# Optimization experiments

Measured on AMD Instinct MI355X. Metric: run time of the kernel, lower is better.

## Reference

```python
import jax, jax.numpy as jnp
import numpy as np

NEG_SLOPE = 0.01  # F.leaky_relu default
EPS = 1e-12       # F.normalize default eps

def _lrelu(h):
    return jnp.where(h > 0, h, NEG_SLOPE * h)

def setup_inputs() -> dict:
    key = jax.random.key(0)
    ks = jax.random.split(key, 16)
    N, E, D = 100000, 800000, 64
    x = jax.random.normal(ks[0], (N, D), dtype=jnp.float32)
    src = jax.random.randint(ks[1], (E,), 0, N, dtype=jnp.int32)
    dst = jax.random.randint(ks[2], (E,), 0, N, dtype=jnp.int32)
    def lin(k, fo, fi):
        k1, k2 = jax.random.split(k)
        s = 1.0 / np.sqrt(fi)
        w = jax.random.uniform(k1, (fo, fi), jnp.float32, -s, s)
        b = jax.random.uniform(k2, (fo,), jnp.float32, -s, s)
        return w, b
    w1, b1 = lin(ks[3], 256, D)
    w2, b2 = lin(ks[4], 128, 256)
    w3, b3 = lin(ks[5], 64, 128)
    w4, b4 = lin(ks[6], 1, 64)
    w_self, _ = lin(ks[7], D, D)   # SAGEConv fc_self (no bias)
    w_neigh, _ = lin(ks[8], D, D)  # SAGEConv fc_neigh (no bias)
    bias = jnp.zeros((D,), jnp.float32)  # SAGEConv bias param
    return dict(x=x, src=src, dst=dst, w1=w1, b1=b1, w2=w2, b2=b2,
                w3=w3, b3=b3, w4=w4, b4=b4,
                w_self=w_self, w_neigh=w_neigh, bias=bias)

def reference(x, src, dst, w1, b1, w2, b2, w3, b3, w4, b4, w_self, w_neigh, bias):
    N = x.shape[0]
    # per-edge score MLP on (h_u - h_v)
    d = x[src] - x[dst]                       # [E, D]
    h = _lrelu(d @ w1.T + b1)                 # [E, 256]
    h = _lrelu(h @ w2.T + b2)                 # [E, 128]
    h = _lrelu(h @ w3.T + b3)                 # [E, 64]
    e = jax.nn.sigmoid(h @ w4.T + b4)         # [E, 1]
    # SAGEConv 'mean' with edge weights: mean over incoming edges of e * x_src
    msg = e * x[src]                          # [E, D]
    s = jax.ops.segment_sum(msg, dst, num_segments=N)               # [N, D]
    deg = jax.ops.segment_sum(jnp.ones((src.shape[0],), x.dtype), dst,
                              num_segments=N)                        # [N]
    neigh = s / jnp.maximum(deg, 1.0)[:, None]
    A = x @ w_self.T + neigh @ w_neigh.T + bias
    A = _lrelu(A)
    norm = jnp.maximum(jnp.linalg.norm(A, axis=1, keepdims=True), EPS)
    A = A / norm
    return A, e
```

## Files before the change

kernel.cpp:

```cpp
#include <hip/hip_runtime.h>
#include <hip/hip_bf16.h>

typedef unsigned short u16;
typedef unsigned int   u32;
typedef __attribute__((ext_vector_type(8))) short short8;
typedef __attribute__((ext_vector_type(4))) float f32x4;

__device__ __forceinline__ u16 f2bf(float f) {
  u32 u = __float_as_uint(f);
  u += 0x7FFFu + ((u >> 16) & 1u);
  return (u16)(u >> 16);
}
__device__ __forceinline__ float bf2f(u16 h) { return __uint_as_float(((u32)h) << 16); }
__device__ __forceinline__ u32 pk2(float lo, float hi) {
  union { __hip_bfloat162 h; u32 u; } c;
  c.h = __float22bfloat162_rn(make_float2(lo, hi));
  return c.u;
}
__device__ __forceinline__ float lrelu(float v) { return v > 0.f ? v : 0.01f * v; }

__host__ __device__ __forceinline__ int sig(int c) {
  return ((c >> 5) << 5) | ((c & 12) << 1) | (((c >> 4) & 1) << 2) | (c & 3);
}

union U8 { u32 w[4]; short8 v; };

#define MFMA16(A, B, C) __builtin_amdgcn_mfma_f32_16x16x32_bf16(A, B, C, 0, 0, 0)

#define W2_BASE 2048
#define W3_BASE 6144
#define NCHUNK8 7168


__global__ __launch_bounds__(512, 1) void edge_mlp(
    const float* __restrict__ x, const int* __restrict__ src, const int* __restrict__ dst,
    const short8* __restrict__ wcat,
    const float* __restrict__ b1p, const float* __restrict__ b2p, const float* __restrict__ b3p,
    const float* __restrict__ w4p, const float* __restrict__ b4,
    const int* __restrict__ rowptr, const int* __restrict__ ord,
    u16* __restrict__ msgbuf, float* __restrict__ eout, int E)
{
  __shared__ short8 ldsw[NCHUNK8];
  const int tid  = threadIdx.x;
  const int lane = tid & 63;
  const int wv   = tid >> 6;
  const int g    = lane >> 4;
  const int r    = lane & 15;
  const int eb   = (blockIdx.x * 8 + wv) * 64;
  const float b4v = b4[0];

  int e[4], ec[4], sn[4], dn[4], pos[4];
#pragma unroll
  for (int c = 0; c < 4; c++) {
    e[c]  = eb + 16 * c + r;
    ec[c] = e[c] < E ? e[c] : E - 1;
    sn[c] = src[ec[c]];
    dn[c] = dst[ec[c]];
  }

  float4 xs[4][4], xd[4][4];
#pragma unroll
  for (int c = 0; c < 4; c++) {
    const float* xsr = x + (size_t)sn[c] * 64 + 8 * g;
    const float* xdr = x + (size_t)dn[c] * 64 + 8 * g;
    xs[c][0] = *(const float4*)(xsr);      xs[c][1] = *(const float4*)(xsr + 4);
    xs[c][2] = *(const float4*)(xsr + 32); xs[c][3] = *(const float4*)(xsr + 36);
    xd[c][0] = *(const float4*)(xdr);      xd[c][1] = *(const float4*)(xdr + 4);
    xd[c][2] = *(const float4*)(xdr + 32); xd[c][3] = *(const float4*)(xdr + 36);
  }
#pragma unroll
  for (int c = 0; c < 4; c++) pos[c] = rowptr[dn[c]] + ord[ec[c]];

  {
    const short8* gp = wcat + wv * 64 + lane;
    short8*       lp = ldsw + wv * 64;
#pragma unroll
    for (int i = 0; i < 14; i++) {
      __builtin_amdgcn_global_load_lds(
          (const __attribute__((address_space(1))) u32*)(gp + i * 512),
          (__attribute__((address_space(3))) u32*)(lp + i * 512), 16, 0, 0);
    }
  }
  __syncthreads();

  U8 bA[4], bB[4];
#pragma unroll
  for (int c = 0; c < 4; c++) {
    bA[c].w[0] = pk2(xs[c][0].x - xd[c][0].x, xs[c][0].y - xd[c][0].y);
    bA[c].w[1] = pk2(xs[c][0].z - xd[c][0].z, xs[c][0].w - xd[c][0].w);
    bA[c].w[2] = pk2(xs[c][1].x - xd[c][1].x, xs[c][1].y - xd[c][1].y);
    bA[c].w[3] = pk2(xs[c][1].z - xd[c][1].z, xs[c][1].w - xd[c][1].w);
    bB[c].w[0] = pk2(xs[c][2].x - xd[c][2].x, xs[c][2].y - xd[c][2].y);
    bB[c].w[1] = pk2(xs[c][2].z - xd[c][2].z, xs[c][2].w - xd[c][2].w);
    bB[c].w[2] = pk2(xs[c][3].x - xd[c][3].x, xs[c][3].y - xd[c][3].y);
    bB[c].w[3] = pk2(xs[c][3].z - xd[c][3].z, xs[c][3].w - xd[c][3].w);
  }

  U8 h1[4][8];
  {
    const float* b1l = b1p + 4 * g;
#pragma unroll
    for (int t = 0; t < 16; t++) {
      short8 a0 = ldsw[(t * 2 + 0) * 64 + lane];
      short8 a1 = ldsw[(t * 2 + 1) * 64 + lane];
      float4 bb = *(const float4*)(b1l + 16 * t);
      const int w0 = 2 * t, w1 = 2 * t + 1;
#pragma unroll
      for (int c = 0; c < 4; c++) {
        f32x4 p = {};
        p = MFMA16(a0, bA[c].v, p);
        p = MFMA16(a1, bB[c].v, p);
        h1[c][w0 >> 2].w[w0 & 3] = pk2(lrelu(p[0] + bb.x), lrelu(p[1] + bb.y));
        h1[c][w1 >> 2].w[w1 & 3] = pk2(lrelu(p[2] + bb.z), lrelu(p[3] + bb.w));
      }
    }
  }

  U8 h2[4][4];
  {
    const float* b2l = b2p + 4 * g;
#pragma unroll
    for (int t = 0; t < 8; t++) {
      f32x4 p0 = {}, p1 = {}, p2 = {}, p3 = {};
#pragma unroll
      for (int s = 0; s < 8; s++) {
        short8 a = ldsw[W2_BASE + (t * 8 + s) * 64 + lane];
        p0 = MFMA16(a, h1[0][s].v, p0);
        p1 = MFMA16(a, h1[1][s].v, p1);
        p2 = MFMA16(a, h1[2][s].v, p2);
        p3 = MFMA16(a, h1[3][s].v, p3);
      }
      float4 bb = *(const float4*)(b2l + 16 * t);
      const int w0 = 2 * t, w1 = 2 * t + 1;
      h2[0][w0 >> 2].w[w0 & 3] = pk2(lrelu(p0[0] + bb.x), lrelu(p0[1] + bb.y));
      h2[0][w1 >> 2].w[w1 & 3] = pk2(lrelu(p0[2] + bb.z), lrelu(p0[3] + bb.w));
      h2[1][w0 >> 2].w[w0 & 3] = pk2(lrelu(p1[0] + bb.x), lrelu(p1[1] + bb.y));
      h2[1][w1 >> 2].w[w1 & 3] = pk2(lrelu(p1[2] + bb.z), lrelu(p1[3] + bb.w));
      h2[2][w0 >> 2].w[w0 & 3] = pk2(lrelu(p2[0] + bb.x), lrelu(p2[1] + bb.y));
      h2[2][w1 >> 2].w[w1 & 3] = pk2(lrelu(p2[2] + bb.z), lrelu(p2[3] + bb.w));
      h2[3][w0 >> 2].w[w0 & 3] = pk2(lrelu(p3[0] + bb.x), lrelu(p3[1] + bb.y));
      h2[3][w1 >> 2].w[w1 & 3] = pk2(lrelu(p3[2] + bb.z), lrelu(p3[3] + bb.w));
    }
  }

  float dot[4] = {0.f, 0.f, 0.f, 0.f};
  {
    const float* b3l = b3p + 4 * g;
    const float* w4l = w4p + 4 * g;
#pragma unroll
    for (int t = 0; t < 4; t++) {
      f32x4 p0 = {}, p1 = {}, p2 = {}, p3 = {};
#pragma unroll
      for (int s = 0; s < 4; s++) {
        short8 a = ldsw[W3_BASE + (t * 4 + s) * 64 + lane];
        p0 = MFMA16(a, h2[0][s].v, p0);
        p1 = MFMA16(a, h2[1][s].v, p1);
        p2 = MFMA16(a, h2[2][s].v, p2);
        p3 = MFMA16(a, h2[3][s].v, p3);
      }
      float4 bb = *(const float4*)(b3l + 16 * t);
      float4 ww = *(const float4*)(w4l + 16 * t);
      dot[0] += lrelu(p0[0] + bb.x) * ww.x + lrelu(p0[1] + bb.y) * ww.y
              + lrelu(p0[2] + bb.z) * ww.z + lrelu(p0[3] + bb.w) * ww.w;
      dot[1] += lrelu(p1[0] + bb.x) * ww.x + lrelu(p1[1] + bb.y) * ww.y
              + lrelu(p1[2] + bb.z) * ww.z + lrelu(p1[3] + bb.w) * ww.w;
      dot[2] += lrelu(p2[0] + bb.x) * ww.x + lrelu(p2[1] + bb.y) * ww.y
              + lrelu(p2[2] + bb.z) * ww.z + lrelu(p2[3] + bb.w) * ww.w;
      dot[3] += lrelu(p3[0] + bb.x) * ww.x + lrelu(p3[1] + bb.y) * ww.y
              + lrelu(p3[2] + bb.z) * ww.z + lrelu(p3[3] + bb.w) * ww.w;
    }
  }
  float ev[4];
#pragma unroll
  for (int c = 0; c < 4; c++) {
    float d = dot[c];
    d += __shfl_xor(d, 16);
    d += __shfl_xor(d, 32);
    ev[c] = 1.f / (1.f + __expf(-(d + b4v)));
  }

  if (g == 0) {
#pragma unroll
    for (int c = 0; c < 4; c++)
      if (e[c] < E) eout[e[c]] = ev[c];
  }
#pragma unroll
  for (int c = 0; c < 4; c++) {
    if (e[c] < E) {
      const float* xsr = x + (size_t)sn[c] * 64 + 8 * g;
      const float4 v0 = *(const float4*)(xsr);
      const float4 v1 = *(const float4*)(xsr + 4);
      const float4 v2 = *(const float4*)(xsr + 32);
      const float4 v3 = *(const float4*)(xsr + 36);
      u16* mp = msgbuf + (size_t)pos[c] * 64 + g * 16;
      U8 m;
      m.w[0] = pk2(ev[c] * v0.x, ev[c] * v0.y);
      m.w[1] = pk2(ev[c] * v0.z, ev[c] * v0.w);
      m.w[2] = pk2(ev[c] * v1.x, ev[c] * v1.y);
      m.w[3] = pk2(ev[c] * v1.z, ev[c] * v1.w);
      *(short8*)(mp) = m.v;
      m.w[0] = pk2(ev[c] * v2.x, ev[c] * v2.y);
      m.w[1] = pk2(ev[c] * v2.z, ev[c] * v2.w);
      m.w[2] = pk2(ev[c] * v3.x, ev[c] * v3.y);
      m.w[3] = pk2(ev[c] * v3.z, ev[c] * v3.w);
      *(short8*)(mp + 8) = m.v;
    }
  }
}

__global__ void deg_hist(const int* __restrict__ dst, int* __restrict__ degi,
                         int* __restrict__ ord, int E)
{
  const int i = blockIdx.x * 256 + threadIdx.x;
  if (i < E) ord[i] = atomicAdd(&degi[dst[i]], 1);
}

__global__ void scan_part(const int* __restrict__ degi, int* __restrict__ rowptr,
                          int* __restrict__ bsum, int N)
{
  __shared__ int wsum[4];
  const int tid = threadIdx.x, lane = tid & 63, w = tid >> 6;
  const int base = blockIdx.x * 1024 + tid * 4;
  int d0 = 0, d1 = 0, d2 = 0, d3 = 0;
  if (base + 3 < N) {
    int4 v = *(const int4*)(degi + base);
    d0 = v.x; d1 = v.y; d2 = v.z; d3 = v.w;
  } else {
    if (base < N)     d0 = degi[base];
    if (base + 1 < N) d1 = degi[base + 1];
    if (base + 2 < N) d2 = degi[base + 2];
    if (base + 3 < N) d3 = degi[base + 3];
  }
  const int ts = d0 + d1 + d2 + d3;
  int sc = ts;
#pragma unroll
  for (int o = 1; o < 64; o <<= 1) { int v = __shfl_up(sc, o); if (lane >= o) sc += v; }
  if (lane == 63) wsum[w] = sc;
  __syncthreads();
  int woff = 0;
  for (int i = 0; i < w; i++) woff += wsum[i];
  const int ex = woff + sc - ts;
  if (base < N)     rowptr[base]     = ex;
  if (base + 1 < N) rowptr[base + 1] = ex + d0;
  if (base + 2 < N) rowptr[base + 2] = ex + d0 + d1;
  if (base + 3 < N) rowptr[base + 3] = ex + d0 + d1 + d2;
  if (tid == 255) bsum[blockIdx.x] = woff + sc;
}

__global__ void scan_bsum(int* __restrict__ bsum, int nb)
{
  __shared__ int wsum[4];
  const int tid = threadIdx.x, lane = tid & 63, w = tid >> 6;
  const int v = tid < nb ? bsum[tid] : 0;
  int sc = v;
#pragma unroll
  for (int o = 1; o < 64; o <<= 1) { int t = __shfl_up(sc, o); if (lane >= o) sc += t; }
  if (lane == 63) wsum[w] = sc;
  __syncthreads();
  int woff = 0;
  for (int i = 0; i < w; i++) woff += wsum[i];
  if (tid < nb) bsum[tid] = woff + sc - v;
}

__global__ void scan_add(int* __restrict__ rowptr, const int* __restrict__ bsum,
                         int N, int E)
{
  const int base = blockIdx.x * 1024 + threadIdx.x * 4;
  const int off = bsum[blockIdx.x];
#pragma unroll
  for (int i = 0; i < 4; i++)
    if (base + i < N) rowptr[base + i] += off;
  if (blockIdx.x == 0 && threadIdx.x == 0) rowptr[N] = E;
}

__global__ __launch_bounds__(256, 4) void node_agg_mfma(
    const float* __restrict__ x, const u16* __restrict__ msgbuf,
    const int* __restrict__ rowptr, const short8* __restrict__ wfin,
    const float* __restrict__ bias, float* __restrict__ A, int N)
{
  __shared__ short8 ldsW[1024];
  __shared__ float  nbuf[4][16][68];
  const int tid = threadIdx.x, wv = tid >> 6, lane = tid & 63;
  const int g = lane >> 4, r = lane & 15;
  for (int i = tid; i < 1024; i += 256) ldsW[i] = wfin[i];

  const int n0 = (blockIdx.x * 4 + wv) * 16;
  const int nr = (n0 + r) < N ? (n0 + r) : N - 1;
  const float* xp = x + (size_t)nr * 64 + 8 * g;
  const float4 xf0 = *(const float4*)(xp);
  const float4 xf1 = *(const float4*)(xp + 4);
  const float4 xf2 = *(const float4*)(xp + 32);
  const float4 xf3 = *(const float4*)(xp + 36);
  int rp = 0;
  if (lane < 17) rp = rowptr[min(n0 + lane, N)];
  const int cch = (((lane >> 3) & 1) << 5) | ((lane >> 4) << 3) | (lane & 7);
  for (int rr = 0; rr < 16; rr++) {
    const int s = __shfl(rp, rr);
    const int t = __shfl(rp, rr + 1);
    float acc = 0.f;
    for (int j = s; j < t; j += 4) {
      const int j1 = (j + 1 < t) ? j + 1 : j;
      const int j2 = (j + 2 < t) ? j + 2 : j;
      const int j3 = (j + 3 < t) ? j + 3 : j;
      const float v0 = bf2f(msgbuf[(size_t)j  * 64 + lane]);
      const float v1 = bf2f(msgbuf[(size_t)j1 * 64 + lane]);
      const float v2 = bf2f(msgbuf[(size_t)j2 * 64 + lane]);
      const float v3 = bf2f(msgbuf[(size_t)j3 * 64 + lane]);
      const float m1 = (j + 1 < t) ? 1.f : 0.f;
      const float m2 = (j + 2 < t) ? 1.f : 0.f;
      const float m3 = (j + 3 < t) ? 1.f : 0.f;
      acc += v0 + m1 * v1 + m2 * v2 + m3 * v3;
    }
    const float inv = 1.f / fmaxf((float)(t - s), 1.f);
    nbuf[wv][rr][cch] = acc * inv;
  }
  __syncthreads();

  U8 bf0, bf1, bf2q, bf3q;
  bf0.w[0] = pk2(xf0.x, xf0.y); bf0.w[1] = pk2(xf0.z, xf0.w);
  bf0.w[2] = pk2(xf1.x, xf1.y); bf0.w[3] = pk2(xf1.z, xf1.w);
  bf1.w[0] = pk2(xf2.x, xf2.y); bf1.w[1] = pk2(xf2.z, xf2.w);
  bf1.w[2] = pk2(xf3.x, xf3.y); bf1.w[3] = pk2(xf3.z, xf3.w);
  {
    const float* nb = nbuf[wv][r];
    const float4 n0v = *(const float4*)(nb + 8 * g);
    const float4 n1v = *(const float4*)(nb + 8 * g + 4);
    const float4 n2v = *(const float4*)(nb + 32 + 8 * g);
    const float4 n3v = *(const float4*)(nb + 32 + 8 * g + 4);
    bf2q.w[0] = pk2(n0v.x, n0v.y); bf2q.w[1] = pk2(n0v.z, n0v.w);
    bf2q.w[2] = pk2(n1v.x, n1v.y); bf2q.w[3] = pk2(n1v.z, n1v.w);
    bf3q.w[0] = pk2(n2v.x, n2v.y); bf3q.w[1] = pk2(n2v.z, n2v.w);
    bf3q.w[2] = pk2(n3v.x, n3v.y); bf3q.w[3] = pk2(n3v.z, n3v.w);
  }

  f32x4 acct[4] = {};
#pragma unroll
  for (int t = 0; t < 4; t++) {
    acct[t] = MFMA16(ldsW[(t * 4 + 0) * 64 + lane], bf0.v,  acct[t]);
    acct[t] = MFMA16(ldsW[(t * 4 + 1) * 64 + lane], bf1.v,  acct[t]);
    acct[t] = MFMA16(ldsW[(t * 4 + 2) * 64 + lane], bf2q.v, acct[t]);
    acct[t] = MFMA16(ldsW[(t * 4 + 3) * 64 + lane], bf3q.v, acct[t]);
  }

  f32x4 av[4];
  float ss = 0.f;
#pragma unroll
  for (int t = 0; t < 4; t++) {
    const float4 bb = *(const float4*)(bias + 16 * t + 4 * g);
    av[t][0] = lrelu(acct[t][0] + bb.x);
    av[t][1] = lrelu(acct[t][1] + bb.y);
    av[t][2] = lrelu(acct[t][2] + bb.z);
    av[t][3] = lrelu(acct[t][3] + bb.w);
    ss += av[t][0] * av[t][0] + av[t][1] * av[t][1]
        + av[t][2] * av[t][2] + av[t][3] * av[t][3];
  }
  ss += __shfl_xor(ss, 16); ss += __shfl_xor(ss, 32);
  const float rn = 1.f / fmaxf(sqrtf(ss), 1e-12f);
  if (n0 + r < N) {
    float* ap = A + (size_t)(n0 + r) * 64 + 4 * g;
#pragma unroll
    for (int t = 0; t < 4; t++) {
      float4 o;
      o.x = av[t][0] * rn; o.y = av[t][1] * rn;
      o.z = av[t][2] * rn; o.w = av[t][3] * rn;
      *(float4*)(ap + 16 * t) = o;
    }
  }
}

__global__ void convert_w(const float* __restrict__ w1, const float* __restrict__ w2,
                          const float* __restrict__ w3,
                          const float* __restrict__ b1, const float* __restrict__ b2,
                          const float* __restrict__ b3, const float* __restrict__ w4,
                          const float* __restrict__ w_self, const float* __restrict__ w_neigh,
                          u16* __restrict__ wcat, u16* __restrict__ wfin,
                          float* __restrict__ b1p, float* __restrict__ b2p,
                          float* __restrict__ b3p, float* __restrict__ w4p)
{
  const int idx = blockIdx.x * 256 + threadIdx.x;
  if (idx < 57344) {
    const float* w; int K, nsteps, loc;
    if (idx < 16384)      { loc = idx;         w = w1; K = 64;  nsteps = 2; }
    else if (idx < 49152) { loc = idx - 16384; w = w2; K = 256; nsteps = 8; }
    else                  { loc = idx - 49152; w = w3; K = 128; nsteps = 4; }
    const int chunk = loc >> 9;
    const int lane  = (loc >> 3) & 63;
    const int j     = loc & 7;
    const int t = chunk / nsteps, s = chunk % nsteps;
    const int m = sig(t * 16 + (lane & 15));
    const int k = s * 32 + (lane >> 4) * 8 + j;
    wcat[idx] = f2bf(w[m * K + k]);
  } else if (idx < 65536) {
    const int o = idx - 57344;
    const int c = o >> 9, lane = (o >> 3) & 63, j = o & 7;
    const int t = c >> 2, s = c & 3;
    const int m = 16 * t + (lane & 15);
    const int k = 32 * s + ((lane >> 4) << 3) + j;
    wfin[o] = f2bf(k < 64 ? w_self[m * 64 + k] : w_neigh[m * 64 + (k - 64)]);
  }
  if (idx < 256) b1p[idx] = b1[sig(idx)];
  if (idx < 128) b2p[idx] = b2[sig(idx)];
  if (idx < 64)  { b3p[idx] = b3[sig(idx)]; w4p[idx] = w4[sig(idx)]; }
}

extern "C" void kernel_launch(void* const* d_in, const int* in_sizes, int n_in,
                              void* d_out, int out_size, void* d_ws, size_t ws_size,
                              hipStream_t stream)
{
  const float* x       = (const float*)d_in[0];
  const int*   src     = (const int*)d_in[1];
  const int*   dst     = (const int*)d_in[2];
  const float* w1      = (const float*)d_in[3];
  const float* b1      = (const float*)d_in[4];
  const float* w2      = (const float*)d_in[5];
  const float* b2      = (const float*)d_in[6];
  const float* w3      = (const float*)d_in[7];
  const float* b3      = (const float*)d_in[8];
  const float* w4      = (const float*)d_in[9];
  const float* b4      = (const float*)d_in[10];
  const float* w_self  = (const float*)d_in[11];
  const float* w_neigh = (const float*)d_in[12];
  const float* bias    = (const float*)d_in[13];

  const int N = in_sizes[0] / 64;
  const int E = in_sizes[1];

  float* A    = (float*)d_out;
  float* eout = (float*)d_out + (size_t)N * 64;

  char* ws = (char*)d_ws;
  size_t off = 0;
  auto alloc = [&](size_t bytes) {
    void* p = ws + off;
    off = (off + bytes + 255) & ~(size_t)255;
    return p;
  };
  int*    degi   = (int*)alloc((size_t)N * 4);
  int*    rowptr = (int*)alloc((size_t)(N + 1) * 4);
  int*    ord    = (int*)alloc((size_t)E * 4);
  int*    bsum   = (int*)alloc(1024 * 4);
  short8* wcat   = (short8*)alloc((size_t)57344 * 2);
  short8* wfin   = (short8*)alloc((size_t)8192 * 2);
  float*  b1p    = (float*)alloc(256 * 4);
  float*  b2p    = (float*)alloc(128 * 4);
  float*  b3p    = (float*)alloc(64 * 4);
  float*  w4p    = (float*)alloc(64 * 4);
  u16*    msgbuf = (u16*)alloc((size_t)E * 128);

  hipMemsetAsync(degi, 0, (size_t)N * sizeof(int), stream);

  convert_w<<<256, 256, 0, stream>>>(w1, w2, w3, b1, b2, b3, w4, w_self, w_neigh,
                                     (u16*)wcat, (u16*)wfin, b1p, b2p, b3p, w4p);

  deg_hist<<<(E + 255) / 256, 256, 0, stream>>>(dst, degi, ord, E);

  const int nsb = (N + 1023) / 1024;
  scan_part<<<nsb, 256, 0, stream>>>(degi, rowptr, bsum, N);
  scan_bsum<<<1, 256, 0, stream>>>(bsum, nsb);
  scan_add<<<nsb, 256, 0, stream>>>(rowptr, bsum, N, E);

  const int nblk = (E + 511) / 512;
  edge_mlp<<<nblk, 512, 0, stream>>>(x, src, dst, wcat, b1p, b2p, b3p, w4p, b4,
                                     rowptr, ord, msgbuf, eout, E);

  const int nblk2 = (N + 63) / 64;
  node_agg_mfma<<<nblk2, 256, 0, stream>>>(x, msgbuf, rowptr, wfin, bias, A, N);
}
```

Measured before the change: 305.3 us.

## Stream MLP weights from global memory with register prefetch instead of LDS staging

Removes the per-block staging of all MLP weights into shared memory and the block barrier. Each wave now reads weight fragments straight from global memory (L2/L1-cached), prefetching the next fragment into registers while the current MFMAs run. Block size drops from 512 to 256 threads. Biases are folded into the MFMA accumulator initialisation, and leaky ReLU becomes a fmax. The trade is more global/L1 traffic per wave and extra register pressure, in exchange for no LDS fill or barrier and a smaller block that may allow more resident blocks.

```diff
diff --git a/kernel.cpp b/kernel.cpp
--- a/kernel.cpp
+++ b/kernel.cpp
@@ -17,7 +17,7 @@
   c.h = __float22bfloat162_rn(make_float2(lo, hi));
   return c.u;
 }
-__device__ __forceinline__ float lrelu(float v) { return v > 0.f ? v : 0.01f * v; }
+__device__ __forceinline__ float lrelu(float v) { return fmaxf(v, 0.01f * v); }
 
 __host__ __device__ __forceinline__ int sig(int c) {
   return ((c >> 5) << 5) | ((c & 12) << 1) | (((c >> 4) & 1) << 2) | (c & 3);
@@ -29,10 +29,9 @@
 
 #define W2_BASE 2048
 #define W3_BASE 6144
-#define NCHUNK8 7168
-
-
-__global__ __launch_bounds__(512, 1) void edge_mlp(
+
+
+__global__ __launch_bounds__(256, 1) void edge_mlp(
     const float* __restrict__ x, const int* __restrict__ src, const int* __restrict__ dst,
     const short8* __restrict__ wcat,
     const float* __restrict__ b1p, const float* __restrict__ b2p, const float* __restrict__ b3p,
@@ -40,13 +39,12 @@
     const int* __restrict__ rowptr, const int* __restrict__ ord,
     u16* __restrict__ msgbuf, float* __restrict__ eout, int E)
 {
-  __shared__ short8 ldsw[NCHUNK8];
   const int tid  = threadIdx.x;
   const int lane = tid & 63;
   const int wv   = tid >> 6;
   const int g    = lane >> 4;
   const int r    = lane & 15;
-  const int eb   = (blockIdx.x * 8 + wv) * 64;
+  const int eb   = (blockIdx.x * 4 + wv) * 64;
   const float b4v = b4[0];
 
   int e[4], ec[4], sn[4], dn[4], pos[4];
@@ -71,17 +69,8 @@
 #pragma unroll
   for (int c = 0; c < 4; c++) pos[c] = rowptr[dn[c]] + ord[ec[c]];
 
-  {
-    const short8* gp = wcat + wv * 64 + lane;
-    short8*       lp = ldsw + wv * 64;
-#pragma unroll
-    for (int i = 0; i < 14; i++) {
-      __builtin_amdgcn_global_load_lds(
-          (const __attribute__((address_space(1))) u32*)(gp + i * 512),
-          (__attribute__((address_space(3))) u32*)(lp + i * 512), 16, 0, 0);
-    }
-  }
-  __syncthreads();
+  short8 w1f0 = wcat[lane];
+  short8 w1f1 = wcat[64 + lane];
 
   U8 bA[4], bB[4];
 #pragma unroll
@@ -101,73 +90,90 @@
     const float* b1l = b1p + 4 * g;
 #pragma unroll
     for (int t = 0; t < 16; t++) {
-      short8 a0 = ldsw[(t * 2 + 0) * 64 + lane];
-      short8 a1 = ldsw[(t * 2 + 1) * 64 + lane];
+      short8 a0 = w1f0, a1 = w1f1;
+      if (t < 15) {
+        w1f0 = wcat[(2 * t + 2) * 64 + lane];
+        w1f1 = wcat[(2 * t + 3) * 64 + lane];
+      }
       float4 bb = *(const float4*)(b1l + 16 * t);
       const int w0 = 2 * t, w1 = 2 * t + 1;
 #pragma unroll
       for (int c = 0; c < 4; c++) {
-        f32x4 p = {};
+        f32x4 p = {bb.x, bb.y, bb.z, bb.w};
         p = MFMA16(a0, bA[c].v, p);
         p = MFMA16(a1, bB[c].v, p);
-        h1[c][w0 >> 2].w[w0 & 3] = pk2(lrelu(p[0] + bb.x), lrelu(p[1] + bb.y));
-        h1[c][w1 >> 2].w[w1 & 3] = pk2(lrelu(p[2] + bb.z), lrelu(p[3] + bb.w));
+        h1[c][w0 >> 2].w[w0 & 3] = pk2(lrelu(p[0]), lrelu(p[1]));
+        h1[c][w1 >> 2].w[w1 & 3] = pk2(lrelu(p[2]), lrelu(p[3]));
       }
     }
   }
 
   U8 h2[4][4];
   {
+    short8 wf0 = wcat[W2_BASE + lane];
+    short8 wf1 = wcat[W2_BASE + 64 + lane];
     const float* b2l = b2p + 4 * g;
 #pragma unroll
     for (int t = 0; t < 8; t++) {
-      f32x4 p0 = {}, p1 = {}, p2 = {}, p3 = {};
-#pragma unroll
-      for (int s = 0; s < 8; s++) {
-        short8 a = ldsw[W2_BASE + (t * 8 + s) * 64 + lane];
-        p0 = MFMA16(a, h1[0][s].v, p0);
-        p1 = MFMA16(a, h1[1][s].v, p1);
-        p2 = MFMA16(a, h1[2][s].v, p2);
-        p3 = MFMA16(a, h1[3][s].v, p3);
+      float4 bb = *(const float4*)(b2l + 16 * t);
+      f32x4 p0 = {bb.x, bb.y, bb.z, bb.w};
+      f32x4 p1 = p0, p2 = p0, p3 = p0;
+#pragma unroll
+      for (int s = 0; s < 8; s += 2) {
+        const int f = t * 8 + s;
+        short8 a0 = wf0, a1 = wf1;
+        if (f + 2 < 64) wf0 = wcat[W2_BASE + (f + 2) * 64 + lane];
+        if (f + 3 < 64) wf1 = wcat[W2_BASE + (f + 3) * 64 + lane];
+        p0 = MFMA16(a0, h1[0][s].v, p0);
+        p1 = MFMA16(a0, h1[1][s].v, p1);
+        p2 = MFMA16(a0, h1[2][s].v, p2);
+        p3 = MFMA16(a0, h1[3][s].v, p3);
+        p0 = MFMA16(a1, h1[0][s + 1].v, p0);
+        p1 = MFMA16(a1, h1[1][s + 1].v, p1);
+        p2 = MFMA16(a1, h1[2][s + 1].v, p2);
+        p3 = MFMA16(a1, h1[3][s + 1].v, p3);
       }
-      float4 bb = *(const float4*)(b2l + 16 * t);
       const int w0 = 2 * t, w1 = 2 * t + 1;
-      h2[0][w0 >> 2].w[w0 & 3] = pk2(lrelu(p0[0] + bb.x), lrelu(p0[1] + bb.y));
-      h2[0][w1 >> 2].w[w1 & 3] = pk2(lrelu(p0[2] + bb.z), lrelu(p0[3] + bb.w));
-      h2[1][w0 >> 2].w[w0 & 3] = pk2(lrelu(p1[0] + bb.x), lrelu(p1[1] + bb.y));
-      h2[1][w1 >> 2].w[w1 & 3] = pk2(lrelu(p1[2] + bb.z), lrelu(p1[3] + bb.w));
-      h2[2][w0 >> 2].w[w0 & 3] = pk2(lrelu(p2[0] + bb.x), lrelu(p2[1] + bb.y));
-      h2[2][w1 >> 2].w[w1 & 3] = pk2(lrelu(p2[2] + bb.z), lrelu(p2[3] + bb.w));
-      h2[3][w0 >> 2].w[w0 & 3] = pk2(lrelu(p3[0] + bb.x), lrelu(p3[1] + bb.y));
-      h2[3][w1 >> 2].w[w1 & 3] = pk2(lrelu(p3[2] + bb.z), lrelu(p3[3] + bb.w));
+      h2[0][w0 >> 2].w[w0 & 3] = pk2(lrelu(p0[0]), lrelu(p0[1]));
+      h2[0][w1 >> 2].w[w1 & 3] = pk2(lrelu(p0[2]), lrelu(p0[3]));
+      h2[1][w0 >> 2].w[w0 & 3] = pk2(lrelu(p1[0]), lrelu(p1[1]));
+      h2[1][w1 >> 2].w[w1 & 3] = pk2(lrelu(p1[2]), lrelu(p1[3]));
+      h2[2][w0 >> 2].w[w0 & 3] = pk2(lrelu(p2[0]), lrelu(p2[1]));
+      h2[2][w1 >> 2].w[w1 & 3] = pk2(lrelu(p2[2]), lrelu(p2[3]));
+      h2[3][w0 >> 2].w[w0 & 3] = pk2(lrelu(p3[0]), lrelu(p3[1]));
+      h2[3][w1 >> 2].w[w1 & 3] = pk2(lrelu(p3[2]), lrelu(p3[3]));
     }
   }
 
   float dot[4] = {0.f, 0.f, 0.f, 0.f};
   {
+    short8 w3f = wcat[W3_BASE + lane];
     const float* b3l = b3p + 4 * g;
     const float* w4l = w4p + 4 * g;
 #pragma unroll
     for (int t = 0; t < 4; t++) {
-      f32x4 p0 = {}, p1 = {}, p2 = {}, p3 = {};
+      float4 bb = *(const float4*)(b3l + 16 * t);
+      f32x4 p0 = {bb.x, bb.y, bb.z, bb.w};
+      f32x4 p1 = p0, p2 = p0, p3 = p0;
 #pragma unroll
       for (int s = 0; s < 4; s++) {
-        short8 a = ldsw[W3_BASE + (t * 4 + s) * 64 + lane];
+        const int cc = t * 4 + s;
+        short8 a = w3f;
+        if (cc < 15) w3f = wcat[W3_BASE + (cc + 1) * 64 + lane];
         p0 = MFMA16(a, h2[0][s].v, p0);
         p1 = MFMA16(a, h2[1][s].v, p1);
         p2 = MFMA16(a, h2[2][s].v, p2);
         p3 = MFMA16(a, h2[3][s].v, p3);
       }
-      float4 bb = *(const float4*)(b3l + 16 * t);
       float4 ww = *(const float4*)(w4l + 16 * t);
-      dot[0] += lrelu(p0[0] + bb.x) * ww.x + lrelu(p0[1] + bb.y) * ww.y
-              + lrelu(p0[2] + bb.z) * ww.z + lrelu(p0[3] + bb.w) * ww.w;
-      dot[1] += lrelu(p1[0] + bb.x) * ww.x + lrelu(p1[1] + bb.y) * ww.y
-              + lrelu(p1[2] + bb.z) * ww.z + lrelu(p1[3] + bb.w) * ww.w;
-      dot[2] += lrelu(p2[0] + bb.x) * ww.x + lrelu(p2[1] + bb.y) * ww.y
-              + lrelu(p2[2] + bb.z) * ww.z + lrelu(p2[3] + bb.w) * ww.w;
-      dot[3] += lrelu(p3[0] + bb.x) * ww.x + lrelu(p3[1] + bb.y) * ww.y
-              + lrelu(p3[2] + bb.z) * ww.z + lrelu(p3[3] + bb.w) * ww.w;
+      dot[0] += lrelu(p0[0]) * ww.x + lrelu(p0[1]) * ww.y
+              + lrelu(p0[2]) * ww.z + lrelu(p0[3]) * ww.w;
+      dot[1] += lrelu(p1[0]) * ww.x + lrelu(p1[1]) * ww.y
+              + lrelu(p1[2]) * ww.z + lrelu(p1[3]) * ww.w;
+      dot[2] += lrelu(p2[0]) * ww.x + lrelu(p2[1]) * ww.y
+              + lrelu(p2[2]) * ww.z + lrelu(p2[3]) * ww.w;
+      dot[3] += lrelu(p3[0]) * ww.x + lrelu(p3[1]) * ww.y
+              + lrelu(p3[2]) * ww.z + lrelu(p3[3]) * ww.w;
     }
   }
   float ev[4];
@@ -459,8 +465,8 @@
   scan_bsum<<<1, 256, 0, stream>>>(bsum, nsb);
   scan_add<<<nsb, 256, 0, stream>>>(rowptr, bsum, N, E);
 
-  const int nblk = (E + 511) / 512;
-  edge_mlp<<<nblk, 512, 0, stream>>>(x, src, dst, wcat, b1p, b2p, b3p, w4p, b4,
+  const int nblk = (E + 255) / 256;
+  edge_mlp<<<nblk, 256, 0, stream>>>(x, src, dst, wcat, b1p, b2p, b3p, w4p, b4,
                                      rowptr, ord, msgbuf, eout, E);
 
   const int nblk2 = (N + 63) / 64;
```

Result: no change. 308.0 us (+0.9%).
